# Kernel tuning notes

Hardware: AMD Instinct MI355X
Metric: run time of the kernel (lower is better)

## Reference

```python
import jax, jax.numpy as jnp
import numpy as np

Q_MAX = 127.0          # 2**(8-1) - 1
QUANTILE = 0.99
GAMMA_MIN, GAMMA_MAX = 0.1, 10.0


def setup_inputs() -> dict:
    key = jax.random.key(0)
    k1, _ = jax.random.split(key)
    x = jax.random.normal(k1, (4, 4096, 2048), dtype=jnp.float32)
    gamma = jnp.ones((1,), dtype=jnp.float32)
    return {"x": x, "gamma": gamma}


def reference(x, gamma):
    # --- quantile of |x| (torch: x.flatten().abs().sort().values[k]) ---
    n = x.size
    k = int(round(QUANTILE * n))
    x_abs = jnp.abs(x.ravel())
    # faithful to full-sort-then-index (the kernel-headroom target)
    q_quantile = jax.lax.stop_gradient(jnp.sort(x_abs)[k])

    # first call: buffer initialized to q_quantile, then EMA with itself
    # -> effective running quantile == q_quantile on this step.
    gamma_c = jnp.clip(gamma, GAMMA_MIN, GAMMA_MAX)  # in-place data clamp in torch
    scale = (q_quantile / Q_MAX) * gamma_c            # shape (1,)

    # omniquant: affine fake-quantize with straight-through estimator
    xq = jnp.clip(jnp.round(x / scale), -Q_MAX - 1.0, Q_MAX) * scale
    out = x + jax.lax.stop_gradient(xq - x)           # STE
    return out
```

## Files before the change

kernel.cpp:

```cpp
#include <hip/hip_runtime.h>
#include <math.h>

typedef unsigned int u32;
typedef float nfloat4 __attribute__((ext_vector_type(4)));


__global__ __launch_bounds__(1024) void hist_top(const u32* __restrict__ x,
                                                 u32* __restrict__ g1,
                                                 long long n) {
  __shared__ u32 h[2048 * 8];
  const int t = threadIdx.x;
  for (int i = t; i < 2048 * 8; i += 1024) h[i] = 0;
  __syncthreads();

  const u32 r = (u32)(t & 7);
  const long long n4 = n >> 2;
  const long long stride = (long long)gridDim.x * 1024;
  const uint4* x4 = (const uint4*)x;
  for (long long i = (long long)blockIdx.x * 1024 + t; i < n4; i += stride) {
    uint4 v = x4[i];
    atomicAdd(&h[(((v.x & 0x7fffffffu) >> 20) << 3) + r], 1u);
    atomicAdd(&h[(((v.y & 0x7fffffffu) >> 20) << 3) + r], 1u);
    atomicAdd(&h[(((v.z & 0x7fffffffu) >> 20) << 3) + r], 1u);
    atomicAdd(&h[(((v.w & 0x7fffffffu) >> 20) << 3) + r], 1u);
  }
  for (long long i = (n4 << 2) + (long long)blockIdx.x * 1024 + t; i < n;
       i += stride) {
    atomicAdd(&h[(((x[i] & 0x7fffffffu) >> 20) << 3) + r], 1u);
  }
  __syncthreads();
  for (int i = t; i < 2048; i += 1024) {
    u32 c = 0;
#pragma unroll
    for (int j = 0; j < 8; ++j) c += h[(i << 3) + j];
    if (c) atomicAdd(&g1[i], c);
  }
}

__global__ __launch_bounds__(1024) void scan_top(const u32* __restrict__ g1,
                                                 u32* __restrict__ sc,
                                                 long long k_in) {
  __shared__ u32 s[1024];
  const int t = threadIdx.x;
  uint2 c2 = ((const uint2*)g1)[t];
  const u32 sum = c2.x + c2.y;
  s[t] = sum;
  __syncthreads();
  for (int off = 1; off < 1024; off <<= 1) {
    u32 add = (t >= off) ? s[t - off] : 0u;
    __syncthreads();
    s[t] += add;
    __syncthreads();
  }
  u32 ex = s[t] - sum;
  const u32 k = (u32)k_in;
  u32 cnt[2] = {c2.x, c2.y};
  for (int i = 0; i < 2; ++i) {
    if (k >= ex && k < ex + cnt[i]) {
      sc[0] = (u32)(t * 2 + i);
      sc[1] = k - ex;
    }
    ex += cnt[i];
  }
}

__global__ __launch_bounds__(1024) void hist_low(const u32* __restrict__ x,
                                                 const u32* __restrict__ sc,
                                                 u32* __restrict__ g2,
                                                 long long n) {
  const u32 B1 = sc[0];
  const int t = threadIdx.x;
  const long long n4 = n >> 2;
  const long long stride = (long long)gridDim.x * 1024;
  const uint4* x4 = (const uint4*)x;
  for (long long i = (long long)blockIdx.x * 1024 + t; i < n4; i += stride) {
    uint4 v = x4[i];
    u32 a;
    a = v.x & 0x7fffffffu; if ((a >> 20) == B1) atomicAdd(&g2[a & 0xFFFFFu], 1u);
    a = v.y & 0x7fffffffu; if ((a >> 20) == B1) atomicAdd(&g2[a & 0xFFFFFu], 1u);
    a = v.z & 0x7fffffffu; if ((a >> 20) == B1) atomicAdd(&g2[a & 0xFFFFFu], 1u);
    a = v.w & 0x7fffffffu; if ((a >> 20) == B1) atomicAdd(&g2[a & 0xFFFFFu], 1u);
  }
  for (long long i = (n4 << 2) + (long long)blockIdx.x * 1024 + t; i < n;
       i += stride) {
    u32 a = x[i] & 0x7fffffffu;
    if ((a >> 20) == B1) atomicAdd(&g2[a & 0xFFFFFu], 1u);
  }
}

__global__ __launch_bounds__(256) void chunk_reduce(const u32* __restrict__ g2,
                                                    u32* __restrict__ cs) {
  const int t = threadIdx.x;
  uint4 v = ((const uint4*)(g2 + (size_t)blockIdx.x * 1024))[t];
  u32 sum = v.x + v.y + v.z + v.w;
#pragma unroll
  for (int off = 32; off > 0; off >>= 1) sum += __shfl_down(sum, off, 64);
  __shared__ u32 w[4];
  if ((t & 63) == 0) w[t >> 6] = sum;
  __syncthreads();
  if (t == 0) cs[blockIdx.x] = w[0] + w[1] + w[2] + w[3];
}

__global__ __launch_bounds__(1024) void scan_low_final(
    const u32* __restrict__ g2, const u32* __restrict__ cs,
    const float* __restrict__ gamma, u32* __restrict__ sc) {
  __shared__ u32 s[1024];
  __shared__ u32 sChunk, sK2;
  const int t = threadIdx.x;
  const u32 B1 = sc[0];
  const u32 krem = sc[1];

  const u32 sum = cs[t];
  s[t] = sum;
  __syncthreads();
  for (int off = 1; off < 1024; off <<= 1) {
    u32 add = (t >= off) ? s[t - off] : 0u;
    __syncthreads();
    s[t] += add;
    __syncthreads();
  }
  u32 ex = s[t] - sum;
  if (krem >= ex && krem < ex + sum) {
    sChunk = (u32)t;
    sK2 = krem - ex;
  }
  __syncthreads();
  const u32 c = sChunk;
  const u32 k2 = sK2;

  const u32 cnt = g2[(size_t)c * 1024 + t];
  __syncthreads();
  s[t] = cnt;
  __syncthreads();
  for (int off = 1; off < 1024; off <<= 1) {
    u32 add = (t >= off) ? s[t - off] : 0u;
    __syncthreads();
    s[t] += add;
    __syncthreads();
  }
  ex = s[t] - cnt;
  if (k2 >= ex && k2 < ex + cnt) {
    const u32 bits = (B1 << 20) | (c * 1024u + (u32)t);
    const float q = __uint_as_float(bits);
    float g = gamma[0];
    g = fminf(fmaxf(g, 0.1f), 10.0f);
    const float scale = (q / 127.0f) * g;
    ((float*)sc)[2] = scale;
  }
}

__global__ __launch_bounds__(256) void quantize(const float* __restrict__ x,
                                                float* __restrict__ out,
                                                const u32* __restrict__ sc,
                                                long long n) {
  const float scale = ((const float*)sc)[2];
  const long long n4 = n >> 2;
  const long long stride = (long long)gridDim.x * 256;
  const float4* x4 = (const float4*)x;
  nfloat4* o4 = (nfloat4*)out;
  for (long long i = (long long)blockIdx.x * 256 + threadIdx.x; i < n4;
       i += stride) {
    float4 v = x4[i];
    nfloat4 o;
    {
      float r = rintf(v.x / scale);
      r = fminf(fmaxf(r, -128.0f), 127.0f);
      o.x = r * scale;
    }
    {
      float r = rintf(v.y / scale);
      r = fminf(fmaxf(r, -128.0f), 127.0f);
      o.y = r * scale;
    }
    {
      float r = rintf(v.z / scale);
      r = fminf(fmaxf(r, -128.0f), 127.0f);
      o.z = r * scale;
    }
    {
      float r = rintf(v.w / scale);
      r = fminf(fmaxf(r, -128.0f), 127.0f);
      o.w = r * scale;
    }
    __builtin_nontemporal_store(o, &o4[i]);
  }
  for (long long i = (n4 << 2) + (long long)blockIdx.x * 256 + threadIdx.x;
       i < n; i += stride) {
    float v = x[i];
    float r = rintf(v / scale);
    r = fminf(fmaxf(r, -128.0f), 127.0f);
    out[i] = r * scale;
  }
}

extern "C" void kernel_launch(void* const* d_in, const int* in_sizes, int n_in,
                              void* d_out, int out_size, void* d_ws,
                              size_t ws_size, hipStream_t stream) {
  const u32* xbits = (const u32*)d_in[0];
  const float* gamma = (const float*)d_in[1];
  const long long n = (long long)in_sizes[0];

  u32* h1 = (u32*)d_ws;
  u32* sc = h1 + 2048;
  u32* cs = sc + 8;
  u32* h2 = (u32*)d_out;

  const long long k = llround(0.99 * (double)n);

  (void)hipMemsetAsync(d_ws, 0, (2048 + 8) * sizeof(u32), stream);
  (void)hipMemsetAsync(d_out, 0, (size_t)(1u << 20) * sizeof(u32), stream);

  hist_top<<<512, 1024, 0, stream>>>(xbits, h1, n);
  scan_top<<<1, 1024, 0, stream>>>(h1, sc, k);
  hist_low<<<512, 1024, 0, stream>>>(xbits, sc, h2, n);
  chunk_reduce<<<1024, 256, 0, stream>>>(h2, cs);
  scan_low_final<<<1, 1024, 0, stream>>>(h2, cs, gamma, sc);
  quantize<<<2048, 256, 0, stream>>>((const float*)d_in[0], (float*)d_out, sc,
                                     n);
}
```

Measured before the change: 287.5 us.

## Replace 20-bit global histogram with candidate compaction and two 10-bit radix passes

The second selection pass no longer builds a 2^20-bin global histogram with global atomics. Each block instead compacts its candidates from the chosen top bucket into a per-block slot buffer, and two small 10-bit radix histogram stages over those candidates then find the exact quantile. The top-bucket scan and the final scans are folded into the histogram kernels using a last-block-done atomic counter, which removes separate single-block kernels and the 4 MB memset. The risk is that the per-block candidate cap (2048 slots) silently drops candidates if a block ever finds more than that in the selected bucket, which would give a wrong quantile.

```diff
diff --git a/kernel.cpp b/kernel.cpp
--- a/kernel.cpp
+++ b/kernel.cpp
@@ -2,12 +2,28 @@
 #include <math.h>
 
 typedef unsigned int u32;
+typedef unsigned long long u64;
 typedef float nfloat4 __attribute__((ext_vector_type(4)));
 
+#define AL(p) __hip_atomic_load((p), __ATOMIC_RELAXED, __HIP_MEMORY_SCOPE_AGENT)
+
+
+#define G1 0
+#define SC 2048
+#define TK 2064
+#define G2 2068
+#define G3 3092
+#define WC 4116
+#define ZERO_U32 4116
+
+#define NSLOT 2048
+#define NBLK_HIST 512
 
 __global__ __launch_bounds__(1024) void hist_top(const u32* __restrict__ x,
-                                                 u32* __restrict__ g1,
-                                                 long long n) {
+                                                 u32* __restrict__ ws,
+                                                 long long n, u32 k) {
+  u32* g1 = ws + G1;
+  u32* sc = ws + SC;
   __shared__ u32 h[2048 * 8];
   const int t = threadIdx.x;
   for (int i = t; i < 2048 * 8; i += 1024) h[i] = 0;
@@ -25,9 +41,8 @@
     atomicAdd(&h[(((v.w & 0x7fffffffu) >> 20) << 3) + r], 1u);
   }
   for (long long i = (n4 << 2) + (long long)blockIdx.x * 1024 + t; i < n;
-       i += stride) {
+       i += stride)
     atomicAdd(&h[(((x[i] & 0x7fffffffu) >> 20) << 3) + r], 1u);
-  }
   __syncthreads();
   for (int i = t; i < 2048; i += 1024) {
     u32 c = 0;
@@ -35,15 +50,20 @@
     for (int j = 0; j < 8; ++j) c += h[(i << 3) + j];
     if (c) atomicAdd(&g1[i], c);
   }
-}
-
-__global__ __launch_bounds__(1024) void scan_top(const u32* __restrict__ g1,
-                                                 u32* __restrict__ sc,
-                                                 long long k_in) {
-  __shared__ u32 s[1024];
-  const int t = threadIdx.x;
-  uint2 c2 = ((const uint2*)g1)[t];
-  const u32 sum = c2.x + c2.y;
+  __threadfence();
+  __syncthreads();
+  __shared__ u32 isLast;
+  if (t == 0) {
+    u32 done = __hip_atomic_fetch_add(ws + TK, 1u, __ATOMIC_ACQ_REL,
+                                      __HIP_MEMORY_SCOPE_AGENT);
+    isLast = (done == (u32)(gridDim.x - 1));
+  }
+  __syncthreads();
+  if (!isLast) return;
+  u32* s = h;
+  const u32 c0 = AL(&g1[2 * t]);
+  const u32 c1 = AL(&g1[2 * t + 1]);
+  const u32 sum = c0 + c1;
   s[t] = sum;
   __syncthreads();
   for (int off = 1; off < 1024; off <<= 1) {
@@ -53,107 +73,139 @@
     __syncthreads();
   }
   u32 ex = s[t] - sum;
-  const u32 k = (u32)k_in;
-  u32 cnt[2] = {c2.x, c2.y};
-  for (int i = 0; i < 2; ++i) {
-    if (k >= ex && k < ex + cnt[i]) {
-      sc[0] = (u32)(t * 2 + i);
-      sc[1] = k - ex;
-    }
-    ex += cnt[i];
-  }
-}
-
-__global__ __launch_bounds__(1024) void hist_low(const u32* __restrict__ x,
-                                                 const u32* __restrict__ sc,
-                                                 u32* __restrict__ g2,
-                                                 long long n) {
-  const u32 B1 = sc[0];
+  if (k >= ex && k < ex + c0) { sc[0] = 2 * t; sc[1] = k - ex; }
+  ex += c0;
+  if (k >= ex && k < ex + c1) { sc[0] = 2 * t + 1; sc[1] = k - ex; }
+}
+
+__global__ __launch_bounds__(1024) void compact(const u32* __restrict__ x,
+                                                u32* __restrict__ ws,
+                                                u32* __restrict__ cand,
+                                                long long n) {
+  const u32 B1 = ws[SC + 0];
+  __shared__ u32 lcnt;
   const int t = threadIdx.x;
+  if (t == 0) lcnt = 0;
+  __syncthreads();
+  u32* slot = cand + (size_t)blockIdx.x * NSLOT;
+  const u32 lane = (u32)(t & 63);
+  const u64 lmask = (1ull << lane) - 1ull;
+
   const long long n4 = n >> 2;
   const long long stride = (long long)gridDim.x * 1024;
   const uint4* x4 = (const uint4*)x;
   for (long long i = (long long)blockIdx.x * 1024 + t; i < n4; i += stride) {
     uint4 v = x4[i];
-    u32 a;
-    a = v.x & 0x7fffffffu; if ((a >> 20) == B1) atomicAdd(&g2[a & 0xFFFFFu], 1u);
-    a = v.y & 0x7fffffffu; if ((a >> 20) == B1) atomicAdd(&g2[a & 0xFFFFFu], 1u);
-    a = v.z & 0x7fffffffu; if ((a >> 20) == B1) atomicAdd(&g2[a & 0xFFFFFu], 1u);
-    a = v.w & 0x7fffffffu; if ((a >> 20) == B1) atomicAdd(&g2[a & 0xFFFFFu], 1u);
+    u32 a[4] = {v.x & 0x7fffffffu, v.y & 0x7fffffffu, v.z & 0x7fffffffu,
+                v.w & 0x7fffffffu};
+#pragma unroll
+    for (int j = 0; j < 4; ++j) {
+      const bool p = (a[j] >> 20) == B1;
+      const u64 m = __ballot(p);
+      if (m) {
+        u32 wbase = 0;
+        if (lane == 0) wbase = atomicAdd(&lcnt, (u32)__popcll(m));
+        wbase = __shfl((int)wbase, 0, 64);
+        if (p) {
+          u32 w = wbase + (u32)__popcll(m & lmask);
+          if (w < NSLOT) slot[w] = a[j] & 0xFFFFFu;
+        }
+      }
+    }
   }
   for (long long i = (n4 << 2) + (long long)blockIdx.x * 1024 + t; i < n;
        i += stride) {
     u32 a = x[i] & 0x7fffffffu;
-    if ((a >> 20) == B1) atomicAdd(&g2[a & 0xFFFFFu], 1u);
-  }
-}
-
-__global__ __launch_bounds__(256) void chunk_reduce(const u32* __restrict__ g2,
-                                                    u32* __restrict__ cs) {
+    if ((a >> 20) == B1) {
+      u32 w = atomicAdd(&lcnt, 1u);
+      if (w < NSLOT) slot[w] = a & 0xFFFFFu;
+    }
+  }
+  __syncthreads();
+  if (t == 0) ws[WC + blockIdx.x] = (lcnt < NSLOT) ? lcnt : NSLOT;
+}
+
+template <int PHASE>
+__global__ __launch_bounds__(256) void select_stage(
+    const u32* __restrict__ cand, u32* __restrict__ ws,
+    const float* __restrict__ gamma) {
+  u32* g = ws + (PHASE == 0 ? G2 : G3);
+  u32* sc = ws + SC;
+  const u32* wcnt = ws + WC;
+  __shared__ u32 h[1024];
   const int t = threadIdx.x;
-  uint4 v = ((const uint4*)(g2 + (size_t)blockIdx.x * 1024))[t];
-  u32 sum = v.x + v.y + v.z + v.w;
-#pragma unroll
-  for (int off = 32; off > 0; off >>= 1) sum += __shfl_down(sum, off, 64);
-  __shared__ u32 w[4];
-  if ((t & 63) == 0) w[t >> 6] = sum;
-  __syncthreads();
-  if (t == 0) cs[blockIdx.x] = w[0] + w[1] + w[2] + w[3];
-}
-
-__global__ __launch_bounds__(1024) void scan_low_final(
-    const u32* __restrict__ g2, const u32* __restrict__ cs,
-    const float* __restrict__ gamma, u32* __restrict__ sc) {
-  __shared__ u32 s[1024];
-  __shared__ u32 sChunk, sK2;
-  const int t = threadIdx.x;
-  const u32 B1 = sc[0];
-  const u32 krem = sc[1];
-
-  const u32 sum = cs[t];
+#pragma unroll
+  for (int i = t; i < 1024; i += 256) h[i] = 0;
+  __syncthreads();
+  const u32 B2 = sc[2];
+  const int total = NBLK_HIST * NSLOT;
+  const int stride = gridDim.x * 256;
+  for (int idx = blockIdx.x * 256 + t; idx < total; idx += stride) {
+    const int slot = idx >> 11, pos = idx & (NSLOT - 1);
+    if ((u32)pos < wcnt[slot]) {
+      const u32 v = cand[idx];
+      if (PHASE == 0)
+        atomicAdd(&h[(v >> 10) & 1023u], 1u);
+      else if (((v >> 10) & 1023u) == B2)
+        atomicAdd(&h[v & 1023u], 1u);
+    }
+  }
+  __syncthreads();
+#pragma unroll
+  for (int i = t; i < 1024; i += 256) {
+    u32 c = h[i];
+    if (c) atomicAdd(&g[i], c);
+  }
+  __threadfence();
+  __syncthreads();
+  __shared__ u32 isLast;
+  if (t == 0) {
+    u32 done = __hip_atomic_fetch_add(ws + TK + 1 + PHASE, 1u,
+                                      __ATOMIC_ACQ_REL,
+                                      __HIP_MEMORY_SCOPE_AGENT);
+    isLast = (done == (u32)(gridDim.x - 1));
+  }
+  __syncthreads();
+  if (!isLast) return;
+  __shared__ u32 s[256];
+  u32 c[4];
+#pragma unroll
+  for (int j = 0; j < 4; ++j) c[j] = AL(&g[4 * t + j]);
+  const u32 sum = c[0] + c[1] + c[2] + c[3];
   s[t] = sum;
   __syncthreads();
-  for (int off = 1; off < 1024; off <<= 1) {
+  for (int off = 1; off < 256; off <<= 1) {
     u32 add = (t >= off) ? s[t - off] : 0u;
     __syncthreads();
     s[t] += add;
     __syncthreads();
   }
   u32 ex = s[t] - sum;
-  if (krem >= ex && krem < ex + sum) {
-    sChunk = (u32)t;
-    sK2 = krem - ex;
-  }
-  __syncthreads();
-  const u32 c = sChunk;
-  const u32 k2 = sK2;
-
-  const u32 cnt = g2[(size_t)c * 1024 + t];
-  __syncthreads();
-  s[t] = cnt;
-  __syncthreads();
-  for (int off = 1; off < 1024; off <<= 1) {
-    u32 add = (t >= off) ? s[t - off] : 0u;
-    __syncthreads();
-    s[t] += add;
-    __syncthreads();
-  }
-  ex = s[t] - cnt;
-  if (k2 >= ex && k2 < ex + cnt) {
-    const u32 bits = (B1 << 20) | (c * 1024u + (u32)t);
-    const float q = __uint_as_float(bits);
-    float g = gamma[0];
-    g = fminf(fmaxf(g, 0.1f), 10.0f);
-    const float scale = (q / 127.0f) * g;
-    ((float*)sc)[2] = scale;
+  const u32 kk = (PHASE == 0) ? sc[1] : sc[3];
+#pragma unroll
+  for (int j = 0; j < 4; ++j) {
+    if (kk >= ex && kk < ex + c[j]) {
+      if (PHASE == 0) {
+        sc[2] = (u32)(4 * t + j);
+        sc[3] = kk - ex;
+      } else {
+        const u32 bits = (sc[0] << 20) | (sc[2] << 10) | (u32)(4 * t + j);
+        const float q = __uint_as_float(bits);
+        float gm = gamma[0];
+        gm = fminf(fmaxf(gm, 0.1f), 10.0f);
+        const float scale = (q / 127.0f) * gm;
+        sc[4] = __float_as_uint(scale);
+      }
+    }
+    ex += c[j];
   }
 }
 
 __global__ __launch_bounds__(256) void quantize(const float* __restrict__ x,
                                                 float* __restrict__ out,
-                                                const u32* __restrict__ sc,
+                                                const u32* __restrict__ ws,
                                                 long long n) {
-  const float scale = ((const float*)sc)[2];
+  const float scale = __uint_as_float(ws[SC + 4]);
   const long long n4 = n >> 2;
   const long long stride = (long long)gridDim.x * 256;
   const float4* x4 = (const float4*)x;
@@ -162,34 +214,16 @@
        i += stride) {
     float4 v = x4[i];
     nfloat4 o;
-    {
-      float r = rintf(v.x / scale);
-      r = fminf(fmaxf(r, -128.0f), 127.0f);
-      o.x = r * scale;
-    }
-    {
-      float r = rintf(v.y / scale);
-      r = fminf(fmaxf(r, -128.0f), 127.0f);
-      o.y = r * scale;
-    }
-    {
-      float r = rintf(v.z / scale);
-      r = fminf(fmaxf(r, -128.0f), 127.0f);
-      o.z = r * scale;
-    }
-    {
-      float r = rintf(v.w / scale);
-      r = fminf(fmaxf(r, -128.0f), 127.0f);
-      o.w = r * scale;
-    }
+    o.x = fminf(fmaxf(rintf(v.x / scale), -128.0f), 127.0f) * scale;
+    o.y = fminf(fmaxf(rintf(v.y / scale), -128.0f), 127.0f) * scale;
+    o.z = fminf(fmaxf(rintf(v.z / scale), -128.0f), 127.0f) * scale;
+    o.w = fminf(fmaxf(rintf(v.w / scale), -128.0f), 127.0f) * scale;
     __builtin_nontemporal_store(o, &o4[i]);
   }
   for (long long i = (n4 << 2) + (long long)blockIdx.x * 256 + threadIdx.x;
        i < n; i += stride) {
     float v = x[i];
-    float r = rintf(v / scale);
-    r = fminf(fmaxf(r, -128.0f), 127.0f);
-    out[i] = r * scale;
+    out[i] = fminf(fmaxf(rintf(v / scale), -128.0f), 127.0f) * scale;
   }
 }
 
@@ -199,22 +233,16 @@
   const u32* xbits = (const u32*)d_in[0];
   const float* gamma = (const float*)d_in[1];
   const long long n = (long long)in_sizes[0];
-
-  u32* h1 = (u32*)d_ws;
-  u32* sc = h1 + 2048;
-  u32* cs = sc + 8;
-  u32* h2 = (u32*)d_out;
-
-  const long long k = llround(0.99 * (double)n);
-
-  (void)hipMemsetAsync(d_ws, 0, (2048 + 8) * sizeof(u32), stream);
-  (void)hipMemsetAsync(d_out, 0, (size_t)(1u << 20) * sizeof(u32), stream);
-
-  hist_top<<<512, 1024, 0, stream>>>(xbits, h1, n);
-  scan_top<<<1, 1024, 0, stream>>>(h1, sc, k);
-  hist_low<<<512, 1024, 0, stream>>>(xbits, sc, h2, n);
-  chunk_reduce<<<1024, 256, 0, stream>>>(h2, cs);
-  scan_low_final<<<1, 1024, 0, stream>>>(h2, cs, gamma, sc);
-  quantize<<<2048, 256, 0, stream>>>((const float*)d_in[0], (float*)d_out, sc,
+  u32* ws = (u32*)d_ws;
+  u32* cand = (u32*)d_out;
+
+  const u32 k = (u32)llround(0.99 * (double)n);
+
+  (void)hipMemsetAsync(ws, 0, ZERO_U32 * sizeof(u32), stream);
+  hist_top<<<NBLK_HIST, 1024, 0, stream>>>(xbits, ws, n, k);
+  compact<<<NBLK_HIST, 1024, 0, stream>>>(xbits, ws, cand, n);
+  select_stage<0><<<128, 256, 0, stream>>>(cand, ws, gamma);
+  select_stage<1><<<128, 256, 0, stream>>>(cand, ws, gamma);
+  quantize<<<2048, 256, 0, stream>>>((const float*)d_in[0], (float*)d_out, ws,
                                      n);
 }
```

Measured after the change: 458.5 us. 1.59x slower.
